# Optimization experiments

Hardware: AMD Instinct MI355X
Metric: run time of the kernel (lower is better)

The kernel has to match this reference:

```python
import jax, jax.numpy as jnp
from jax import lax
import numpy as np

S2 = float(1.0 / np.sqrt(2.0))


def _haar_base():
    # matches create_wavelet_filter('db1') after the [::-1]/flip manipulations
    lo = jnp.array([S2, S2], jnp.float32)
    hi = jnp.array([S2, -S2], jnp.float32)
    # f[k][i,j]: [lo_i*lo_j, hi_i*lo_j, lo_i*hi_j, hi_i*hi_j]
    return jnp.stack([lo[:, None] * lo[None, :], hi[:, None] * lo[None, :],
                      lo[:, None] * hi[None, :], hi[:, None] * hi[None, :]], 0)  # (4,2,2)


def _conv(x, w, stride=1, pad=0, groups=1, lhs_dil=1):
    return lax.conv_general_dilated(
        x, w, (stride, stride), [(pad, pad), (pad, pad)],
        lhs_dilation=(lhs_dil, lhs_dil),
        dimension_numbers=('NCHW', 'OIHW', 'NCHW'),
        feature_group_count=groups)


def _wt(x, c):
    # grouped stride-2 Haar decompose: (b,c,h,w) -> (b,c,4,h/2,w/2)
    w = jnp.tile(_haar_base()[:, None], (c, 1, 1, 1))  # (4c,1,2,2)
    b, _, h, ww = x.shape
    y = _conv(x, w, stride=2, pad=0, groups=c)
    return y.reshape(b, c, 4, h // 2, ww // 2)


def _iwt(x, c):
    # conv_transpose2d(stride=2, groups=c, pad=0) == lhs-dilated conv with flipped kernel, pad=k-1
    base = _haar_base()[:, ::-1, ::-1]           # spatial flip, (4,2,2)
    w = jnp.tile(base[None], (c, 1, 1, 1))       # (c,4,2,2)
    b, _, _, hh, ww = x.shape
    return _conv(x.reshape(b, c * 4, hh, ww), w, stride=1, pad=1, groups=c, lhs_dil=2)


def _reflect(coord, size):
    m = float(size - 1)
    if m <= 0:
        return jnp.zeros_like(coord)
    period = 2.0 * m
    c = jnp.abs(coord) % period
    return jnp.where(c > m, period - c, c)


def _grid_sample_reflect(img, px, py):
    # bilinear grid_sample, padding_mode='reflection', align_corners=True
    # img (b,c,h,w); px,py (b,h,w) absolute pixel coords
    b, c, h, w = img.shape
    px = jnp.clip(_reflect(px, w), 0.0, w - 1)
    py = jnp.clip(_reflect(py, h), 0.0, h - 1)
    x0 = jnp.floor(px); y0 = jnp.floor(py)
    fx = (px - x0)[..., None]; fy = (py - y0)[..., None]
    x0i = jnp.clip(x0.astype(jnp.int32), 0, w - 1)
    y0i = jnp.clip(y0.astype(jnp.int32), 0, h - 1)
    x1i = jnp.clip(x0i + 1, 0, w - 1)
    y1i = jnp.clip(y0i + 1, 0, h - 1)
    t = img.transpose(0, 2, 3, 1)  # (b,h,w,c)
    bi = jnp.arange(b)[:, None, None]
    v00 = t[bi, y0i, x0i]; v01 = t[bi, y0i, x1i]
    v10 = t[bi, y1i, x0i]; v11 = t[bi, y1i, x1i]
    out = (v00 * (1 - fx) + v01 * fx) * (1 - fy) + (v10 * (1 - fx) + v11 * fx) * fy
    return out.transpose(0, 3, 1, 2)


def _dysnake(x, off_w, off_b, dw_w, k=3):
    b, c, h, w = x.shape
    off = _conv(x, off_w, pad=k // 2) + off_b[None, :, None, None]  # (b,2k,h,w)
    ox = off[:, :k].mean(1)   # (b,h,w)
    oy = off[:, k:].mean(1)
    # normalize-then-unnormalize with align_corners=True is identity -> absolute coords
    px = jnp.arange(w, dtype=x.dtype)[None, None, :] + ox
    py = jnp.arange(h, dtype=x.dtype)[None, :, None] + oy
    xd = _grid_sample_reflect(x, px, py)
    return jax.nn.relu(_conv(xd, dw_w, pad=1, groups=c))


def _forward(x, base_w, base_b, base_scale, levels):
    c = x.shape[1]
    ll_list, h_list, shapes = [], [], []
    cur = x
    for (ow, ob, dw, pw, ws) in levels:
        sh = cur.shape
        shapes.append(sh)
        if sh[2] % 2 or sh[3] % 2:
            cur = jnp.pad(cur, ((0, 0), (0, 0), (0, sh[2] % 2), (0, sh[3] % 2)))
        cx = _wt(cur, c)              # (b,c,4,hh,ww)
        cur = cx[:, :, 0]
        b_, _, _, hh, ww = cx.shape
        tag = cx.reshape(b_, c * 4, hh, ww)
        tag = _dysnake(tag, ow, ob, dw)
        tag = _conv(tag, pw, groups=c)   # grouped 1x1
        tag = (ws * tag).reshape(b_, c, 4, hh, ww)
        ll_list.append(tag[:, :, 0])
        h_list.append(tag[:, :, 1:4])
    nxt = jnp.zeros((), x.dtype)
    for i in range(len(levels) - 1, -1, -1):
        ll = ll_list[i] + nxt
        cx = jnp.concatenate([ll[:, :, None], h_list[i]], axis=2)
        nxt = _iwt(cx, c)
        sh = shapes[i]
        nxt = nxt[:, :, :sh[2], :sh[3]]
    base = base_scale * (_conv(x, base_w, pad=1, groups=c) + base_b[None, :, None, None])
    return base + nxt


def setup_inputs() -> dict:
    key = jax.random.key(0)
    ks = jax.random.split(key, 16)
    b, c, h, w = 16, 64, 128, 128
    d = {}
    d['x'] = jax.random.normal(ks[0], (b, c, h, w), jnp.float32)
    d['base_w'] = jax.random.normal(ks[1], (c, 1, 3, 3), jnp.float32) * 0.1
    d['base_b'] = jax.random.normal(ks[2], (c,), jnp.float32) * 0.1
    d['base_scale'] = jnp.ones((1, c, 1, 1), jnp.float32)
    for i in range(2):
        d[f'off_w{i}'] = jax.random.normal(ks[3 + 5 * i], (6, 4 * c, 3, 3), jnp.float32) * 0.01
        d[f'off_b{i}'] = jax.random.normal(ks[4 + 5 * i], (6,), jnp.float32) * 0.01
        d[f'dw_w{i}'] = jax.random.normal(ks[5 + 5 * i], (4 * c, 1, 3, 3), jnp.float32) * 0.1
        d[f'pw_w{i}'] = jax.random.normal(ks[6 + 5 * i], (4 * c, 4, 1, 1), jnp.float32) * 0.1
        d[f'wscale{i}'] = jnp.full((1, 4 * c, 1, 1), 0.1, jnp.float32)
    return d


def reference(x, base_w, base_b, base_scale,
              off_w0, off_b0, dw_w0, pw_w0, wscale0,
              off_w1, off_b1, dw_w1, pw_w1, wscale1):
    levels = [(off_w0, off_b0, dw_w0, pw_w0, wscale0),
              (off_w1, off_b1, dw_w1, pw_w1, wscale1)]
    return _forward(x, base_w, base_b, base_scale, levels)
```

## Files before the change

kernel.cpp:

```cpp
#include <hip/hip_runtime.h>

typedef _Float16 half4 __attribute__((ext_vector_type(4)));
typedef _Float16 half8 __attribute__((ext_vector_type(8), aligned(8)));

static __device__ __forceinline__ half4 to_h4(float4 v) {
    half4 h; h.x = (_Float16)v.x; h.y = (_Float16)v.y; h.z = (_Float16)v.z; h.w = (_Float16)v.w; return h;
}
static __device__ __forceinline__ float4 to_f4(half4 h) {
    return make_float4((float)h.x, (float)h.y, (float)h.z, (float)h.w);
}
static __device__ __forceinline__ float4 f4lo(half8 h) {
    return make_float4((float)h[0], (float)h[1], (float)h[2], (float)h[3]);
}
static __device__ __forceinline__ float4 f4hi(half8 h) {
    return make_float4((float)h[4], (float)h[5], (float)h[6], (float)h[7]);
}
static __device__ __forceinline__ half4 h4splat(float v) {
    _Float16 h = (_Float16)v; half4 r = { h, h, h, h }; return r;
}

static __device__ __forceinline__ float reflectf(float coord, float m) {
    float period = 2.0f * m;
    float c = fmodf(fabsf(coord), period);
    c = (c > m) ? (period - c) : c;
    return fminf(fmaxf(c, 0.0f), m);
}

__global__ __launch_bounds__(256) void k_wt01(
    const float* __restrict__ x, half4* __restrict__ tag0v, half4* __restrict__ tag1v,
    const float* __restrict__ offw0, const float* __restrict__ offb0,
    const float* __restrict__ offw1, const float* __restrict__ offb1,
    float* __restrict__ avgw, float* __restrict__ avgb) {
    int id = blockIdx.x * 256 + threadIdx.x;
    if (id < 2 * 2 * 2304) {
        int l = id / 4608;
        int rem = id % 4608;
        int d = rem / 2304;
        int r = rem % 2304;
        const float* w = l ? offw1 : offw0;
        float s = w[(d * 3 + 0) * 2304 + r] + w[(d * 3 + 1) * 2304 + r] + w[(d * 3 + 2) * 2304 + r];
        avgw[id] = s * (1.0f / 3.0f);
        if (id == 0) {
            avgb[0] = (offb0[0] + offb0[1] + offb0[2]) * (1.0f / 3.0f);
            avgb[1] = (offb0[3] + offb0[4] + offb0[5]) * (1.0f / 3.0f);
            avgb[2] = (offb1[0] + offb1[1] + offb1[2]) * (1.0f / 3.0f);
            avgb[3] = (offb1[3] + offb1[4] + offb1[5]) * (1.0f / 3.0f);
        }
    }
    if (id >= 16 * 64 * 32 * 32) return;
    int j1 = id & 31; int t = id >> 5;
    int i1 = t & 31; t >>= 5;
    int c = t & 63; int b = t >> 6;
    const float* p = x + ((long)(b * 64 + c) * 128 + 4 * i1) * 128 + 4 * j1;
    float4 r0 = *(const float4*)p;
    float4 r1 = *(const float4*)(p + 128);
    float4 r2 = *(const float4*)(p + 256);
    float4 r3 = *(const float4*)(p + 384);
    #define HAAR(a0,a1,a2,a3) make_float4(0.5f*((a0)+(a1)+(a2)+(a3)), 0.5f*((a0)+(a1)-(a2)-(a3)), \
                                          0.5f*((a0)-(a1)+(a2)-(a3)), 0.5f*((a0)-(a1)-(a2)+(a3)))
    float4 t00 = HAAR(r0.x, r0.y, r1.x, r1.y);
    float4 t01 = HAAR(r0.z, r0.w, r1.z, r1.w);
    float4 t10 = HAAR(r2.x, r2.y, r3.x, r3.y);
    float4 t11 = HAAR(r2.z, r2.w, r3.z, r3.w);
    long pbase = (long)(b * 64 + c) * 4096;
    int i0 = 2 * i1, j0 = 2 * j1;
    tag0v[pbase + (long)i0 * 64 + j0]           = to_h4(t00);
    tag0v[pbase + (long)i0 * 64 + j0 + 1]       = to_h4(t01);
    tag0v[pbase + (long)(i0 + 1) * 64 + j0]     = to_h4(t10);
    tag0v[pbase + (long)(i0 + 1) * 64 + j0 + 1] = to_h4(t11);
    tag1v[(long)(b * 64 + c) * 1024 + (long)i1 * 32 + j1] = to_h4(HAAR(t00.x, t01.x, t10.x, t11.x));
    #undef HAAR
}

__global__ __launch_bounds__(256) void k_off_part_both(
    const half4* __restrict__ tag0, const half4* __restrict__ tag1,
    const float* __restrict__ avgw,
    _Float16* __restrict__ part0, _Float16* __restrict__ part1) {
    int bx = blockIdx.x;
    const half4* tagv; _Float16* part; int level, hh, ww;
    if (bx < 128) { tagv = tag0; part = part0; level = 0; hh = 64; ww = 64; }
    else          { bx -= 128; tagv = tag1; part = part1; level = 1; hh = 32; ww = 32; }
    int chunk = blockIdx.y;
    int npix = hh * ww;
    int totpix = 16 * npix;
    __shared__ float wls[2][4][9][4];
    const float* wsrc = avgw + level * 4608;
    int tid = threadIdx.x;
    for (int t = tid; t < 288; t += 256) {
        int d = t / 144, rem = t % 144;
        int gg = rem / 36; int tap = (rem % 36) / 4; int cc = rem & 3;
        wls[d][gg][tap][cc] = wsrc[d * 2304 + (chunk * 16 + gg * 4 + cc) * 9 + tap];
    }
    __syncthreads();
    int id2 = bx * 256 + tid;
    if (id2 >= (totpix >> 1)) return;
    int wwh = ww >> 1;
    int jp = (id2 % wwh) * 2;
    int t2 = id2 / wwh;
    int i = t2 % hh; int b = t2 / hh;
    float ax0 = 0.f, ay0 = 0.f, ax1 = 0.f, ay1 = 0.f;
    const float4 z4 = make_float4(0.f, 0.f, 0.f, 0.f);
    #pragma unroll
    for (int gg = 0; gg < 4; gg++) {
        const half4* pg = tagv + ((long)b * 64 + chunk * 4 + gg) * npix;
        half8 hL0, hL1, hL2, hR0, hR1, hR2;
        int y0 = i - 1, y1 = i, y2 = i + 1;
        bool r0ok = (unsigned)y0 < (unsigned)hh;
        bool r2ok = (unsigned)y2 < (unsigned)hh;
        int jl = (jp == 0) ? 0 : jp - 1;
        {
            int yc0 = r0ok ? y0 : 0, yc2 = r2ok ? y2 : 0;
            hL0 = *(const half8*)(pg + yc0 * ww + jl);
            hR0 = *(const half8*)(pg + yc0 * ww + jp + 1);
            hL1 = *(const half8*)(pg + y1 * ww + jl);
            hR1 = *(const half8*)(pg + y1 * ww + jp + 1);
            hL2 = *(const half8*)(pg + yc2 * ww + jl);
            hR2 = *(const half8*)(pg + yc2 * ww + jp + 1);
        }
        bool rok[3] = { r0ok, true, r2ok };
        half8 HL[3] = { hL0, hL1, hL2 };
        half8 HR[3] = { hR0, hR1, hR2 };
        bool rimax = (jp + 2 < ww);
        #pragma unroll
        for (int di = 0; di < 3; di++) {
            float4 vm1, v0, v1, v2;
            if (rok[di]) {
                float4 lo = f4lo(HL[di]), hi = f4hi(HL[di]);
                if (jp == 0) { vm1 = z4; v0 = lo; }
                else         { vm1 = lo; v0 = hi; }
                v1 = f4lo(HR[di]);
                v2 = rimax ? f4hi(HR[di]) : z4;
            } else { vm1 = z4; v0 = z4; v1 = z4; v2 = z4; }
            #pragma unroll
            for (int dj = 0; dj < 3; dj++) {
                float4 v = (dj == 0) ? vm1 : (dj == 1) ? v0 : v1;
                const float* wx = &wls[0][gg][di * 3 + dj][0];
                const float* wy = &wls[1][gg][di * 3 + dj][0];
                ax0 = fmaf(v.x, wx[0], ax0); ax0 = fmaf(v.y, wx[1], ax0);
                ax0 = fmaf(v.z, wx[2], ax0); ax0 = fmaf(v.w, wx[3], ax0);
                ay0 = fmaf(v.x, wy[0], ay0); ay0 = fmaf(v.y, wy[1], ay0);
                ay0 = fmaf(v.z, wy[2], ay0); ay0 = fmaf(v.w, wy[3], ay0);
            }
            #pragma unroll
            for (int dj = 0; dj < 3; dj++) {
                float4 v = (dj == 0) ? v0 : (dj == 1) ? v1 : v2;
                const float* wx = &wls[0][gg][di * 3 + dj][0];
                const float* wy = &wls[1][gg][di * 3 + dj][0];
                ax1 = fmaf(v.x, wx[0], ax1); ax1 = fmaf(v.y, wx[1], ax1);
                ax1 = fmaf(v.z, wx[2], ax1); ax1 = fmaf(v.w, wx[3], ax1);
                ay1 = fmaf(v.x, wy[0], ay1); ay1 = fmaf(v.y, wy[1], ay1);
                ay1 = fmaf(v.z, wy[2], ay1); ay1 = fmaf(v.w, wy[3], ay1);
            }
        }
    }
    long pid = (long)b * npix + (long)i * ww + jp;
    part[(long)chunk * totpix + pid]        = (_Float16)ax0;
    part[(long)chunk * totpix + pid + 1]    = (_Float16)ax1;
    part[((long)16 + chunk) * totpix + pid]     = (_Float16)ay0;
    part[((long)16 + chunk) * totpix + pid + 1] = (_Float16)ay1;
}

__global__ __launch_bounds__(256) void k_off_red_both(
    const _Float16* __restrict__ part0, const _Float16* __restrict__ part1,
    const float* __restrict__ avgb,
    float* __restrict__ ox0, float* __restrict__ oy0,
    float* __restrict__ ox1, float* __restrict__ oy1) {
    int bx = blockIdx.x;
    const _Float16* part; float* ox; float* oy; int level, totpix;
    if (bx < 256) { part = part0; ox = ox0; oy = oy0; level = 0; totpix = 65536; }
    else          { bx -= 256; part = part1; ox = ox1; oy = oy1; level = 1; totpix = 16384; }
    int id = bx * 256 + threadIdx.x;
    if (id >= totpix) return;
    float sx = avgb[level * 2 + 0], sy = avgb[level * 2 + 1];
    #pragma unroll
    for (int c = 0; c < 16; c++) sx += (float)part[(long)c * totpix + id];
    #pragma unroll
    for (int c = 0; c < 16; c++) sy += (float)part[((long)16 + c) * totpix + id];
    ox[id] = sx; oy[id] = sy;
}

template<int GPB>
__global__ __launch_bounds__(256) void k_snake(
    const half4* __restrict__ tagv,
    const float* __restrict__ ox, const float* __restrict__ oy,
    const float* __restrict__ dww, const float* __restrict__ pww,
    const float* __restrict__ wsc,
    half4* __restrict__ outv, int B, int hh, int ww) {
    __shared__ half4 sbuf[2][18][19];
    __shared__ half4 dwWh[GPB][9];
    __shared__ float pwW[GPB][16];
    __shared__ float wscW[GPB][4];
    int tilesX = ww >> 4;
    int tile = blockIdx.x;
    int g0 = blockIdx.y * GPB;
    int bz = blockIdx.z;
    int i0 = (tile / tilesX) * 16;
    int j0 = (tile % tilesX) * 16;
    int tid = threadIdx.x;
    for (int t = tid; t < GPB * 36; t += 256) {
        int gg = t / 36, rem = t % 36, cc = rem / 9, tap = rem % 9;
        ((_Float16*)&dwWh[gg][tap])[cc] = (_Float16)dww[g0 * 36 + t];
    }
    for (int t = tid; t < GPB * 16; t += 256) pwW[t / 16][t % 16] = pww[g0 * 16 + t];
    for (int t = tid; t < GPB * 4;  t += 256) wscW[t / 4][t % 4]  = wsc[g0 * 4 + t];
    int npix = hh * ww;
    const float* oxb = ox + (long)bz * npix;
    const float* oyb = oy + (long)bz * npix;
    float mW = (float)(ww - 1), mH = (float)(hh - 1);
    int p0 = tid, p1 = tid + 256;
    bool has1 = (p1 < 324);
    int ty0 = p0 / 18, tx0 = p0 % 18;
    int ty1 = p1 / 18, tx1 = p1 % 18;
    float4 wv0 = make_float4(0.f, 0.f, 0.f, 0.f), wv1 = wv0;
    int4 iv0 = make_int4(0, 0, 0, 0), iv1 = iv0;
    {
        int y = i0 - 1 + ty0, x = j0 - 1 + tx0;
        if (p0 < 324 && (unsigned)y < (unsigned)hh && (unsigned)x < (unsigned)ww) {
            float px = (float)x + oxb[y * ww + x];
            float py = (float)y + oyb[y * ww + x];
            px = reflectf(px, mW); py = reflectf(py, mH);
            float x0f = floorf(px), y0f = floorf(py);
            float fx = px - x0f, fy = py - y0f;
            int x0 = min(max((int)x0f, 0), ww - 1);
            int y0 = min(max((int)y0f, 0), hh - 1);
            int x1 = min(x0 + 1, ww - 1);
            int y1 = min(y0 + 1, hh - 1);
            wv0.x = (1.f - fx) * (1.f - fy); wv0.y = fx * (1.f - fy);
            wv0.z = (1.f - fx) * fy;         wv0.w = fx * fy;
            iv0.x = y0 * ww + x0; iv0.z = y1 * ww + x0; iv0.y = (x1 == x0) ? 1 : 0;
        }
        y = i0 - 1 + ty1; x = j0 - 1 + tx1;
        if (has1 && (unsigned)y < (unsigned)hh && (unsigned)x < (unsigned)ww) {
            float px = (float)x + oxb[y * ww + x];
            float py = (float)y + oyb[y * ww + x];
            px = reflectf(px, mW); py = reflectf(py, mH);
            float x0f = floorf(px), y0f = floorf(py);
            float fx = px - x0f, fy = py - y0f;
            int x0 = min(max((int)x0f, 0), ww - 1);
            int y0 = min(max((int)y0f, 0), hh - 1);
            int x1 = min(x0 + 1, ww - 1);
            int y1 = min(y0 + 1, hh - 1);
            wv1.x = (1.f - fx) * (1.f - fy); wv1.y = fx * (1.f - fy);
            wv1.z = (1.f - fx) * fy;         wv1.w = fx * fy;
            iv1.x = y0 * ww + x0; iv1.z = y1 * ww + x0; iv1.y = (x1 == x0) ? 1 : 0;
        }
    }
    half4 w00h0 = h4splat(wv0.x), w01h0 = h4splat(wv0.y), w10h0 = h4splat(wv0.z), w11h0 = h4splat(wv0.w);
    half4 w00h1 = h4splat(wv1.x), w01h1 = h4splat(wv1.y), w10h1 = h4splat(wv1.z), w11h1 = h4splat(wv1.w);
    half4 a00h, a01h, a10h, a11h, b00h, b01h, b10h, b11h;
    #define ISSUE(g) { const half4* pg = tagv + ((long)bz * 64 + (g)) * npix; \
        half8 hA = *(const half8*)(pg + iv0.x); \
        half8 hB = *(const half8*)(pg + iv0.z); \
        a00h = __builtin_shufflevector(hA, hA, 0, 1, 2, 3); \
        a01h = iv0.y ? a00h : __builtin_shufflevector(hA, hA, 4, 5, 6, 7); \
        a10h = __builtin_shufflevector(hB, hB, 0, 1, 2, 3); \
        a11h = iv0.y ? a10h : __builtin_shufflevector(hB, hB, 4, 5, 6, 7); \
        if (has1) { \
            half8 hC = *(const half8*)(pg + iv1.x); \
            half8 hD = *(const half8*)(pg + iv1.z); \
            b00h = __builtin_shufflevector(hC, hC, 0, 1, 2, 3); \
            b01h = iv1.y ? b00h : __builtin_shufflevector(hC, hC, 4, 5, 6, 7); \
            b10h = __builtin_shufflevector(hD, hD, 0, 1, 2, 3); \
            b11h = iv1.y ? b10h : __builtin_shufflevector(hD, hD, 4, 5, 6, 7); } }
    #define WRITEBUF(nb) { \
        sbuf[nb][ty0][tx0] = a00h * w00h0 + a01h * w01h0 + a10h * w10h0 + a11h * w11h0; \
        if (has1) sbuf[nb][ty1][tx1] = b00h * w00h1 + b01h * w01h1 + b10h * w10h1 + b11h * w11h1; }
    ISSUE(g0);
    WRITEBUF(0);
    __syncthreads();
    int ti = tid >> 4, tj = tid & 15;
    int oi = i0 + ti, oj = j0 + tj;
    long outbase = ((long)bz * 64 + g0) * npix + (long)oi * ww + oj;
    #pragma unroll
    for (int gg = 0; gg < GPB; gg++) {
        const int cur = gg & 1;
        if (gg + 1 < GPB) ISSUE(g0 + gg + 1);
        half4 acch = { (_Float16)0, (_Float16)0, (_Float16)0, (_Float16)0 };
        #pragma unroll
        for (int di = 0; di < 3; di++)
            #pragma unroll
            for (int dj = 0; dj < 3; dj++)
                acch = sbuf[cur][ti + di][tj + dj] * dwWh[gg][di * 3 + dj] + acch;
        float4 accf = to_f4(acch);
        float r0 = fmaxf(accf.x, 0.f), r1 = fmaxf(accf.y, 0.f);
        float r2 = fmaxf(accf.z, 0.f), r3 = fmaxf(accf.w, 0.f);
        float4 o;
        o.x = (r0 * pwW[gg][0]  + r1 * pwW[gg][1]  + r2 * pwW[gg][2]  + r3 * pwW[gg][3])  * wscW[gg][0];
        o.y = (r0 * pwW[gg][4]  + r1 * pwW[gg][5]  + r2 * pwW[gg][6]  + r3 * pwW[gg][7])  * wscW[gg][1];
        o.z = (r0 * pwW[gg][8]  + r1 * pwW[gg][9]  + r2 * pwW[gg][10] + r3 * pwW[gg][11]) * wscW[gg][2];
        o.w = (r0 * pwW[gg][12] + r1 * pwW[gg][13] + r2 * pwW[gg][14] + r3 * pwW[gg][15]) * wscW[gg][3];
        outv[outbase + (long)gg * npix] = to_h4(o);
        if (gg + 1 < GPB) {
            WRITEBUF(cur ^ 1);
            __syncthreads();
        }
    }
    #undef ISSUE
    #undef WRITEBUF
}

__global__ __launch_bounds__(256) void k_snake_final(
    const half4* __restrict__ tagv,
    const half4* __restrict__ tagp1v,
    const float* __restrict__ ox, const float* __restrict__ oy,
    const float* __restrict__ dww, const float* __restrict__ pww,
    const float* __restrict__ wsc,
    const float* __restrict__ x,
    const float* __restrict__ bw, const float* __restrict__ bb,
    const float* __restrict__ bs,
    float* __restrict__ out) {
    const int GPB = 4, hh = 64, ww = 64, npix = 4096;
    __shared__ half4 sbuf[2][18][19];
    __shared__ float xs[2][34][36];
    __shared__ half4 dwWh[GPB][9];
    __shared__ float pwW[GPB][16];
    __shared__ float wscW[GPB][4];
    __shared__ float bwW[GPB][9];
    __shared__ float bbW[GPB];
    __shared__ float bsW[GPB];
    int tile = blockIdx.x;
    int g0 = blockIdx.y * GPB;
    int bz = blockIdx.z;
    int i0 = (tile >> 2) * 16;
    int j0 = (tile & 3) * 16;
    int yy0 = 2 * i0, xx0 = 2 * j0;
    int tid = threadIdx.x;
    for (int t = tid; t < GPB * 36; t += 256) {
        int gg = t / 36, rem = t % 36, cc = rem / 9, tap = rem % 9;
        ((_Float16*)&dwWh[gg][tap])[cc] = (_Float16)dww[g0 * 36 + t];
    }
    for (int t = tid; t < GPB * 16; t += 256) pwW[t / 16][t % 16] = pww[g0 * 16 + t];
    for (int t = tid; t < GPB * 4;  t += 256) wscW[t / 4][t % 4]  = wsc[g0 * 4 + t];
    for (int t = tid; t < GPB * 9;  t += 256) bwW[t / 9][t % 9]   = bw[g0 * 9 + t];
    if (tid < GPB) { bbW[tid] = bb[g0 + tid]; bsW[tid] = bs[g0 + tid]; }
    const float* oxb = ox + (long)bz * npix;
    const float* oyb = oy + (long)bz * npix;
    float mW = 63.f, mH = 63.f;
    int p0 = tid, p1 = tid + 256;
    bool has1 = (p1 < 324);
    int ty0 = p0 / 18, tx0 = p0 % 18;
    int ty1 = p1 / 18, tx1 = p1 % 18;
    float4 wv0 = make_float4(0.f, 0.f, 0.f, 0.f), wv1 = wv0;
    int4 iv0 = make_int4(0, 0, 0, 0), iv1 = iv0;
    {
        int y = i0 - 1 + ty0, xg = j0 - 1 + tx0;
        if ((unsigned)y < (unsigned)hh && (unsigned)xg < (unsigned)ww) {
            float px = (float)xg + oxb[y * ww + xg];
            float py = (float)y + oyb[y * ww + xg];
            px = reflectf(px, mW); py = reflectf(py, mH);
            float x0f = floorf(px), y0f = floorf(py);
            float fx = px - x0f, fy = py - y0f;
            int x0 = min(max((int)x0f, 0), ww - 1);
            int y0 = min(max((int)y0f, 0), hh - 1);
            int x1 = min(x0 + 1, ww - 1);
            int y1 = min(y0 + 1, hh - 1);
            wv0.x = (1.f - fx) * (1.f - fy); wv0.y = fx * (1.f - fy);
            wv0.z = (1.f - fx) * fy;         wv0.w = fx * fy;
            iv0.x = y0 * ww + x0; iv0.z = y1 * ww + x0; iv0.y = (x1 == x0) ? 1 : 0;
        }
        y = i0 - 1 + ty1; xg = j0 - 1 + tx1;
        if (has1 && (unsigned)y < (unsigned)hh && (unsigned)xg < (unsigned)ww) {
            float px = (float)xg + oxb[y * ww + xg];
            float py = (float)y + oyb[y * ww + xg];
            px = reflectf(px, mW); py = reflectf(py, mH);
            float x0f = floorf(px), y0f = floorf(py);
            float fx = px - x0f, fy = py - y0f;
            int x0 = min(max((int)x0f, 0), ww - 1);
            int y0 = min(max((int)y0f, 0), hh - 1);
            int x1 = min(x0 + 1, ww - 1);
            int y1 = min(y0 + 1, hh - 1);
            wv1.x = (1.f - fx) * (1.f - fy); wv1.y = fx * (1.f - fy);
            wv1.z = (1.f - fx) * fy;         wv1.w = fx * fy;
            iv1.x = y0 * ww + x0; iv1.z = y1 * ww + x0; iv1.y = (x1 == x0) ? 1 : 0;
        }
    }
    half4 w00h0 = h4splat(wv0.x), w01h0 = h4splat(wv0.y), w10h0 = h4splat(wv0.z), w11h0 = h4splat(wv0.w);
    half4 w00h1 = h4splat(wv1.x), w01h1 = h4splat(wv1.y), w10h1 = h4splat(wv1.z), w11h1 = h4splat(wv1.w);
    half4 a00h, a01h, a10h, a11h, b00h, b01h, b10h, b11h;
    float xr[5];
    #define ISSUE(g) { const half4* pg = tagv + ((long)bz * 64 + (g)) * npix; \
        half8 hA = *(const half8*)(pg + iv0.x); \
        half8 hB = *(const half8*)(pg + iv0.z); \
        a00h = __builtin_shufflevector(hA, hA, 0, 1, 2, 3); \
        a01h = iv0.y ? a00h : __builtin_shufflevector(hA, hA, 4, 5, 6, 7); \
        a10h = __builtin_shufflevector(hB, hB, 0, 1, 2, 3); \
        a11h = iv0.y ? a10h : __builtin_shufflevector(hB, hB, 4, 5, 6, 7); \
        if (has1) { \
            half8 hC = *(const half8*)(pg + iv1.x); \
            half8 hD = *(const half8*)(pg + iv1.z); \
            b00h = __builtin_shufflevector(hC, hC, 0, 1, 2, 3); \
            b01h = iv1.y ? b00h : __builtin_shufflevector(hC, hC, 4, 5, 6, 7); \
            b10h = __builtin_shufflevector(hD, hD, 0, 1, 2, 3); \
            b11h = iv1.y ? b10h : __builtin_shufflevector(hD, hD, 4, 5, 6, 7); } }
    #define WRITEBUF(nb) { \
        sbuf[nb][ty0][tx0] = a00h * w00h0 + a01h * w01h0 + a10h * w10h0 + a11h * w11h0; \
        if (has1) sbuf[nb][ty1][tx1] = b00h * w00h1 + b01h * w01h1 + b10h * w10h1 + b11h * w11h1; }
    #define XLOAD(c) { const float* xbc = x + (long)(bz * 64 + (c)) * 16384; \
        _Pragma("unroll") \
        for (int q = 0; q < 5; q++) { int p = tid + q * 256; float v = 0.f; \
            if (p < 1156) { int r = p / 34, qq = p % 34; \
                int y = yy0 - 1 + r, xg = xx0 - 1 + qq; \
                if ((unsigned)y < 128u && (unsigned)xg < 128u) v = xbc[y * 128 + xg]; } \
            xr[q] = v; } }
    #define XWRITE(nb) { _Pragma("unroll") \
        for (int q = 0; q < 5; q++) { int p = tid + q * 256; \
            if (p < 1156) xs[nb][p / 34][p % 34] = xr[q]; } }
    ISSUE(g0);
    XLOAD(g0);
    WRITEBUF(0);
    XWRITE(0);
    __syncthreads();
    int ti = tid >> 4, tj = tid & 15;
    int i = i0 + ti, j = j0 + tj;
    int yy = 2 * i, xx = 2 * j;
    float sr = (i & 1) ? -1.f : 1.f;
    float sc = (j & 1) ? -1.f : 1.f;
    long t1base = ((long)(bz * 64)) * 1024 + (long)(i >> 1) * 32 + (j >> 1);
    int a = 2 * ti, bq = 2 * tj;
    #pragma unroll
    for (int gg = 0; gg < GPB; gg++) {
        const int cur = gg & 1;
        if (gg + 1 < GPB) { ISSUE(g0 + gg + 1); XLOAD(g0 + gg + 1); }
        float4 d = to_f4(tagp1v[t1base + (long)(g0 + gg) * 1024]);
        half4 acch = { (_Float16)0, (_Float16)0, (_Float16)0, (_Float16)0 };
        #pragma unroll
        for (int di = 0; di < 3; di++)
            #pragma unroll
            for (int dj = 0; dj < 3; dj++)
                acch = sbuf[cur][ti + di][tj + dj] * dwWh[gg][di * 3 + dj] + acch;
        float4 accf = to_f4(acch);
        float r0 = fmaxf(accf.x, 0.f), r1 = fmaxf(accf.y, 0.f);
        float r2 = fmaxf(accf.z, 0.f), r3 = fmaxf(accf.w, 0.f);
        float4 o;
        o.x = (r0 * pwW[gg][0]  + r1 * pwW[gg][1]  + r2 * pwW[gg][2]  + r3 * pwW[gg][3])  * wscW[gg][0];
        o.y = (r0 * pwW[gg][4]  + r1 * pwW[gg][5]  + r2 * pwW[gg][6]  + r3 * pwW[gg][7])  * wscW[gg][1];
        o.z = (r0 * pwW[gg][8]  + r1 * pwW[gg][9]  + r2 * pwW[gg][10] + r3 * pwW[gg][11]) * wscW[gg][2];
        o.w = (r0 * pwW[gg][12] + r1 * pwW[gg][13] + r2 * pwW[gg][14] + r3 * pwW[gg][15]) * wscW[gg][3];
        float nv = 0.5f * (d.x + sr * d.y + sc * d.z + sr * sc * d.w);
        float c0 = o.x + nv;
        float c1 = o.y, c2 = o.z, c3 = o.w;
        float rec00 = 0.5f * (c0 + c1 + c2 + c3);
        float rec01 = 0.5f * (c0 + c1 - c2 - c3);
        float rec10 = 0.5f * (c0 - c1 + c2 - c3);
        float rec11 = 0.5f * (c0 - c1 - c2 + c3);
        float bias = bbW[gg], scale = bsW[gg];
        float w0 = bwW[gg][0], w1 = bwW[gg][1], w2 = bwW[gg][2];
        float w3 = bwW[gg][3], w4 = bwW[gg][4], w5 = bwW[gg][5];
        float w6 = bwW[gg][6], w7 = bwW[gg][7], w8 = bwW[gg][8];
        float xv[4][4];
        #pragma unroll
        for (int r = 0; r < 4; r++) {
            float2 lo = *(const float2*)&xs[cur][a + r][bq];
            float2 hi = *(const float2*)&xs[cur][a + r][bq + 2];
            xv[r][0] = lo.x; xv[r][1] = lo.y; xv[r][2] = hi.x; xv[r][3] = hi.y;
        }
        #define CONV(dy,dx) ({ \
            float accc = bias; \
            accc = fmaf(xv[dy+0][dx+0], w0, accc); \
            accc = fmaf(xv[dy+0][dx+1], w1, accc); \
            accc = fmaf(xv[dy+0][dx+2], w2, accc); \
            accc = fmaf(xv[dy+1][dx+0], w3, accc); \
            accc = fmaf(xv[dy+1][dx+1], w4, accc); \
            accc = fmaf(xv[dy+1][dx+2], w5, accc); \
            accc = fmaf(xv[dy+2][dx+0], w6, accc); \
            accc = fmaf(xv[dy+2][dx+1], w7, accc); \
            accc = fmaf(xv[dy+2][dx+2], w8, accc); \
            accc; })
        float o00 = scale * CONV(0,0) + rec00;
        float o01 = scale * CONV(0,1) + rec01;
        float o10 = scale * CONV(1,0) + rec10;
        float o11 = scale * CONV(1,1) + rec11;
        #undef CONV
        float* ob = out + (((long)(bz * 64 + g0 + gg) * 128) + yy) * 128 + xx;
        *(float2*)ob         = make_float2(o00, o01);
        *(float2*)(ob + 128) = make_float2(o10, o11);
        if (gg + 1 < GPB) {
            WRITEBUF(cur ^ 1);
            XWRITE(cur ^ 1);
            __syncthreads();
        }
    }
    #undef ISSUE
    #undef WRITEBUF
    #undef XLOAD
    #undef XWRITE
}

extern "C" void kernel_launch(void* const* d_in, const int* in_sizes, int n_in,
                              void* d_out, int out_size, void* d_ws, size_t ws_size,
                              hipStream_t stream) {
    const float* x     = (const float*)d_in[0];
    const float* bw    = (const float*)d_in[1];
    const float* bb    = (const float*)d_in[2];
    const float* bs    = (const float*)d_in[3];
    const float* offw0 = (const float*)d_in[4];
    const float* offb0 = (const float*)d_in[5];
    const float* dww0  = (const float*)d_in[6];
    const float* pww0  = (const float*)d_in[7];
    const float* wsc0  = (const float*)d_in[8];
    const float* offw1 = (const float*)d_in[9];
    const float* offb1 = (const float*)d_in[10];
    const float* dww1  = (const float*)d_in[11];
    const float* pww1  = (const float*)d_in[12];
    const float* wsc1  = (const float*)d_in[13];
    float* out = (float*)d_out;
    float* ws = (float*)d_ws;

    half4*     tag0h  = (half4*)(ws + 0L);
    half4*     tag1h  = (half4*)(ws + 8388608L);
    half4*     tagp1h = (half4*)(ws + 10485760L);
    _Float16*  part0h = (_Float16*)(ws + 12582912L);
    _Float16*  part1h = (_Float16*)(ws + 13631488L);
    float* avgw = ws + 13893632L;
    float* avgb = ws + 13902848L;
    float* ox0  = ws + 13902852L;
    float* oy0  = ws + 13968388L;
    float* ox1  = ws + 14033924L;
    float* oy1  = ws + 14050308L;

    k_wt01<<<4096, 256, 0, stream>>>(x, tag0h, tag1h, offw0, offb0, offw1, offb1, avgw, avgb);
    k_off_part_both<<<dim3(160, 16), 256, 0, stream>>>(tag0h, tag1h, avgw, part0h, part1h);
    k_off_red_both<<<320, 256, 0, stream>>>(part0h, part1h, avgb, ox0, oy0, ox1, oy1);
    k_snake<4><<<dim3(4, 16, 16), 256, 0, stream>>>(tag1h, ox1, oy1, dww1, pww1, wsc1,
                                                    tagp1h, 16, 32, 32);
    k_snake_final<<<dim3(16, 16, 16), 256, 0, stream>>>(
        tag0h, tagp1h, ox0, oy0, dww0, pww0, wsc0,
        x, bw, bb, bs, out);
}
```

Measured before the change: 141.2 us.

## Tile offset-conv partial kernel with shared-memory halo staging

The offset-prediction partial convolution now loads each block's input into shared memory as a 16x16 output tile with a one-pixel halo, across its four channel groups. Each thread then computes one output pixel from shared memory, replacing the previous scheme of two pixels per thread using direct half8 global loads. The goal is to cut redundant global reads of neighbouring pixels and the boundary-handling branches. In exchange it adds a shared-memory staging phase, a barrier, and a 3D launch grid with more, smaller blocks.

```diff
diff --git a/kernel.cpp b/kernel.cpp
--- a/kernel.cpp
+++ b/kernel.cpp
@@ -8,12 +8,6 @@
 }
 static __device__ __forceinline__ float4 to_f4(half4 h) {
     return make_float4((float)h.x, (float)h.y, (float)h.z, (float)h.w);
-}
-static __device__ __forceinline__ float4 f4lo(half8 h) {
-    return make_float4((float)h[0], (float)h[1], (float)h[2], (float)h[3]);
-}
-static __device__ __forceinline__ float4 f4hi(half8 h) {
-    return make_float4((float)h[4], (float)h[5], (float)h[6], (float)h[7]);
 }
 static __device__ __forceinline__ half4 h4splat(float v) {
     _Float16 h = (_Float16)v; half4 r = { h, h, h, h }; return r;
@@ -77,87 +71,56 @@
     const float* __restrict__ avgw,
     _Float16* __restrict__ part0, _Float16* __restrict__ part1) {
     int bx = blockIdx.x;
-    const half4* tagv; _Float16* part; int level, hh, ww;
-    if (bx < 128) { tagv = tag0; part = part0; level = 0; hh = 64; ww = 64; }
-    else          { bx -= 128; tagv = tag1; part = part1; level = 1; hh = 32; ww = 32; }
+    const half4* tagv; _Float16* part; int level, hh, ww, tilesX;
+    if (bx < 16) { tagv = tag0; part = part0; level = 0; hh = 64; ww = 64; tilesX = 4; }
+    else { bx -= 16; tagv = tag1; part = part1; level = 1; hh = 32; ww = 32; tilesX = 2; }
     int chunk = blockIdx.y;
+    int b = blockIdx.z;
     int npix = hh * ww;
     int totpix = 16 * npix;
+    int i0 = (bx / tilesX) * 16, j0 = (bx % tilesX) * 16;
+    __shared__ half4 s[4][18][19];
     __shared__ float wls[2][4][9][4];
+    int tid = threadIdx.x;
     const float* wsrc = avgw + level * 4608;
-    int tid = threadIdx.x;
     for (int t = tid; t < 288; t += 256) {
         int d = t / 144, rem = t % 144;
         int gg = rem / 36; int tap = (rem % 36) / 4; int cc = rem & 3;
         wls[d][gg][tap][cc] = wsrc[d * 2304 + (chunk * 16 + gg * 4 + cc) * 9 + tap];
     }
+    const half4 zh = { (_Float16)0, (_Float16)0, (_Float16)0, (_Float16)0 };
+    for (int p = tid; p < 324; p += 256) {
+        int ty = p / 18, tx = p % 18;
+        int y = i0 - 1 + ty, xg = j0 - 1 + tx;
+        bool ok = (unsigned)y < (unsigned)hh && (unsigned)xg < (unsigned)ww;
+        #pragma unroll
+        for (int gg = 0; gg < 4; gg++) {
+            const half4* pg = tagv + ((long)b * 64 + chunk * 4 + gg) * npix;
+            s[gg][ty][tx] = ok ? pg[y * ww + xg] : zh;
+        }
+    }
     __syncthreads();
-    int id2 = bx * 256 + tid;
-    if (id2 >= (totpix >> 1)) return;
-    int wwh = ww >> 1;
-    int jp = (id2 % wwh) * 2;
-    int t2 = id2 / wwh;
-    int i = t2 % hh; int b = t2 / hh;
-    float ax0 = 0.f, ay0 = 0.f, ax1 = 0.f, ay1 = 0.f;
-    const float4 z4 = make_float4(0.f, 0.f, 0.f, 0.f);
+    int ti = tid >> 4, tj = tid & 15;
+    float ax = 0.f, ay = 0.f;
     #pragma unroll
     for (int gg = 0; gg < 4; gg++) {
-        const half4* pg = tagv + ((long)b * 64 + chunk * 4 + gg) * npix;
-        half8 hL0, hL1, hL2, hR0, hR1, hR2;
-        int y0 = i - 1, y1 = i, y2 = i + 1;
-        bool r0ok = (unsigned)y0 < (unsigned)hh;
-        bool r2ok = (unsigned)y2 < (unsigned)hh;
-        int jl = (jp == 0) ? 0 : jp - 1;
-        {
-            int yc0 = r0ok ? y0 : 0, yc2 = r2ok ? y2 : 0;
-            hL0 = *(const half8*)(pg + yc0 * ww + jl);
-            hR0 = *(const half8*)(pg + yc0 * ww + jp + 1);
-            hL1 = *(const half8*)(pg + y1 * ww + jl);
-            hR1 = *(const half8*)(pg + y1 * ww + jp + 1);
-            hL2 = *(const half8*)(pg + yc2 * ww + jl);
-            hR2 = *(const half8*)(pg + yc2 * ww + jp + 1);
-        }
-        bool rok[3] = { r0ok, true, r2ok };
-        half8 HL[3] = { hL0, hL1, hL2 };
-        half8 HR[3] = { hR0, hR1, hR2 };
-        bool rimax = (jp + 2 < ww);
         #pragma unroll
         for (int di = 0; di < 3; di++) {
-            float4 vm1, v0, v1, v2;
-            if (rok[di]) {
-                float4 lo = f4lo(HL[di]), hi = f4hi(HL[di]);
-                if (jp == 0) { vm1 = z4; v0 = lo; }
-                else         { vm1 = lo; v0 = hi; }
-                v1 = f4lo(HR[di]);
-                v2 = rimax ? f4hi(HR[di]) : z4;
-            } else { vm1 = z4; v0 = z4; v1 = z4; v2 = z4; }
             #pragma unroll
             for (int dj = 0; dj < 3; dj++) {
-                float4 v = (dj == 0) ? vm1 : (dj == 1) ? v0 : v1;
+                float4 v = to_f4(s[gg][ti + di][tj + dj]);
                 const float* wx = &wls[0][gg][di * 3 + dj][0];
                 const float* wy = &wls[1][gg][di * 3 + dj][0];
-                ax0 = fmaf(v.x, wx[0], ax0); ax0 = fmaf(v.y, wx[1], ax0);
-                ax0 = fmaf(v.z, wx[2], ax0); ax0 = fmaf(v.w, wx[3], ax0);
-                ay0 = fmaf(v.x, wy[0], ay0); ay0 = fmaf(v.y, wy[1], ay0);
-                ay0 = fmaf(v.z, wy[2], ay0); ay0 = fmaf(v.w, wy[3], ay0);
+                ax = fmaf(v.x, wx[0], ax); ax = fmaf(v.y, wx[1], ax);
+                ax = fmaf(v.z, wx[2], ax); ax = fmaf(v.w, wx[3], ax);
+                ay = fmaf(v.x, wy[0], ay); ay = fmaf(v.y, wy[1], ay);
+                ay = fmaf(v.z, wy[2], ay); ay = fmaf(v.w, wy[3], ay);
             }
-            #pragma unroll
-            for (int dj = 0; dj < 3; dj++) {
-                float4 v = (dj == 0) ? v0 : (dj == 1) ? v1 : v2;
-                const float* wx = &wls[0][gg][di * 3 + dj][0];
-                const float* wy = &wls[1][gg][di * 3 + dj][0];
-                ax1 = fmaf(v.x, wx[0], ax1); ax1 = fmaf(v.y, wx[1], ax1);
-                ax1 = fmaf(v.z, wx[2], ax1); ax1 = fmaf(v.w, wx[3], ax1);
-                ay1 = fmaf(v.x, wy[0], ay1); ay1 = fmaf(v.y, wy[1], ay1);
-                ay1 = fmaf(v.z, wy[2], ay1); ay1 = fmaf(v.w, wy[3], ay1);
-            }
-        }
-    }
-    long pid = (long)b * npix + (long)i * ww + jp;
-    part[(long)chunk * totpix + pid]        = (_Float16)ax0;
-    part[(long)chunk * totpix + pid + 1]    = (_Float16)ax1;
-    part[((long)16 + chunk) * totpix + pid]     = (_Float16)ay0;
-    part[((long)16 + chunk) * totpix + pid + 1] = (_Float16)ay1;
+        }
+    }
+    long pid = (long)b * npix + (long)(i0 + ti) * ww + (j0 + tj);
+    part[(long)chunk * totpix + pid]        = (_Float16)ax;
+    part[((long)16 + chunk) * totpix + pid] = (_Float16)ay;
 }
 
 __global__ __launch_bounds__(256) void k_off_red_both(
@@ -519,7 +482,7 @@
     float* oy1  = ws + 14050308L;
 
     k_wt01<<<4096, 256, 0, stream>>>(x, tag0h, tag1h, offw0, offb0, offw1, offb1, avgw, avgb);
-    k_off_part_both<<<dim3(160, 16), 256, 0, stream>>>(tag0h, tag1h, avgw, part0h, part1h);
+    k_off_part_both<<<dim3(20, 16, 16), 256, 0, stream>>>(tag0h, tag1h, avgw, part0h, part1h);
     k_off_red_both<<<320, 256, 0, stream>>>(part0h, part1h, avgb, ox0, oy0, ox1, oy1);
     k_snake<4><<<dim3(4, 16, 16), 256, 0, stream>>>(tag1h, ox1, oy1, dww1, pww1, wsc1,
                                                     tagp1h, 16, 32, 32);
```

Result: faster. 116.3 us (-17.7%).
